# Performance work log

Measured on AMD Instinct MI355X. Metric: run time of the kernel, lower is better.

Reference implementation:

```python
import jax, jax.numpy as jnp
import numpy as np

N_NODES = 100000
N_EDGES = 1600000
HIDDEN = 64
IN_CH = 6  # 3 (direction) + 3 (node feature part)
BN_EPS = 1e-5


def setup_inputs() -> dict:
    key = jax.random.key(0)
    ks = jax.random.split(key, 16)
    inp = {
        "x": jax.random.normal(ks[0], (N_NODES, 3), dtype=jnp.float32),
        "pos": jax.random.normal(ks[1], (N_NODES, 3), dtype=jnp.float32),
        "edge_index": jax.random.randint(ks[2], (2, N_EDGES), 0, N_NODES, dtype=jnp.int64),
    }
    dims = [IN_CH, HIDDEN, HIDDEN, HIDDEN]
    for i in range(3):
        din, dout = dims[i], dims[i + 1]
        inp[f"W{i+1}"] = jax.random.normal(ks[3 + 4 * i], (din, dout), dtype=jnp.float32) * (1.0 / np.sqrt(din))
        inp[f"b{i+1}"] = jnp.zeros((dout,), dtype=jnp.float32)
        inp[f"g{i+1}"] = jnp.ones((dout,), dtype=jnp.float32)   # BN gamma
        inp[f"be{i+1}"] = jnp.zeros((dout,), dtype=jnp.float32)  # BN beta
    return inp


def _mlp_layer(h, W, b, g, be):
    # Linear -> ReLU -> BatchNorm1d (training mode, biased variance like torch)
    h = jax.nn.relu(h @ W + b)
    mu = jnp.mean(h, axis=0)
    var = jnp.mean((h - mu) ** 2, axis=0)
    return g * (h - mu) * jax.lax.rsqrt(var + BN_EPS) + be


def reference(x, pos, edge_index, W1, b1, g1, be1, W2, b2, g2, be2, W3, b3, g3, be3):
    n = x.shape[0]
    xp = jnp.concatenate([pos, x], axis=1)             # [N, 3+F]
    src, dst = edge_index[0], edge_index[1]            # j = src, i = dst (PyG source_to_target)
    x_j = xp[src]                                      # [E, 3+F]
    x_i = xp[dst]
    direction = x_j[:, :3] - x_i[:, :3]                # [E, 3]
    # NOTE: source uses torch.norm with no dim => single global scalar norm
    direction = direction / jnp.linalg.norm(direction)
    h = jnp.concatenate([direction, x_i[:, 3:]], axis=-1)  # [E, IN_CH]
    h = _mlp_layer(h, W1, b1, g1, be1)
    h = _mlp_layer(h, W2, b2, g2, be2)
    h = _mlp_layer(h, W3, b3, g3, be3)                 # [E, HIDDEN]
    out = jax.ops.segment_max(h, dst, num_segments=n)  # scatter-max aggregation
    out = jnp.where(jnp.isfinite(out), out, 0.0)       # PyG fills empty segments with 0
    return out
```

## Files before the change

### kernel.cpp

```cpp
#include <hip/hip_runtime.h>
#include <stdint.h>

typedef unsigned char u8;
typedef unsigned short u16;
typedef unsigned int u32;
typedef __attribute__((ext_vector_type(8))) short short8;
typedef __attribute__((ext_vector_type(4))) float floatx4;

#define BN_EPS 1e-5f
#define NPB 64
#define NPB_SHIFT 6
#define NBMAX 2048

__device__ __forceinline__ float bf2f(u16 u) { return __uint_as_float(((unsigned)u) << 16); }
__device__ __forceinline__ u16 f2bf(float f) {
  unsigned u = __float_as_uint(f);
  u += 0x7FFFu + ((u >> 16) & 1u);
  return (u16)(u >> 16);
}

__global__ void k_init(float* __restrict__ stats, u32* __restrict__ bucketTotal) {
  for (int i = threadIdx.x; i < 1024; i += blockDim.x) stats[i] = 0.f;
  for (int i = threadIdx.x; i < NBMAX + 1; i += blockDim.x) bucketTotal[i] = 0u;
}

__global__ void k_norm_hist(const int* __restrict__ ei, const float* __restrict__ pos,
                            int E, int NB, float* __restrict__ stats,
                            u32* __restrict__ bucketTotal) {
  __shared__ u32 lh[NBMAX];
  __shared__ float red[16];
  for (int i = threadIdx.x; i < NB; i += blockDim.x) lh[i] = 0u;
  __syncthreads();
  int tid = blockIdx.x * blockDim.x + threadIdx.x;
  int stride = gridDim.x * blockDim.x;
  float acc = 0.f;
  for (int e = tid; e < E; e += stride) {
    int s = ei[e], d = ei[E + e];
    float d0 = pos[3 * s + 0] - pos[3 * d + 0];
    float d1 = pos[3 * s + 1] - pos[3 * d + 1];
    float d2 = pos[3 * s + 2] - pos[3 * d + 2];
    acc = fmaf(d0, d0, acc);
    acc = fmaf(d1, d1, acc);
    acc = fmaf(d2, d2, acc);
    atomicAdd(&lh[d >> NPB_SHIFT], 1u);
  }
#pragma unroll
  for (int off = 32; off > 0; off >>= 1) acc += __shfl_down(acc, off, 64);
  if ((threadIdx.x & 63) == 0) red[threadIdx.x >> 6] = acc;
  __syncthreads();
  if (threadIdx.x == 0) {
    float s = 0.f;
    for (int w = 0; w < (int)(blockDim.x >> 6); w++) s += red[w];
    atomicAdd(&stats[0], s);
  }
  for (int i = threadIdx.x; i < NB; i += blockDim.x)
    if (lh[i]) atomicAdd(&bucketTotal[i], lh[i]);
}

__global__ void k_scan(const u32* __restrict__ bucketTotal, u32* __restrict__ base,
                       u32* __restrict__ cursor, int NB) {
  int lane = threadIdx.x;
  u32 run = 0;
  for (int b0 = 0; b0 < NB; b0 += 64) {
    int b = b0 + lane;
    u32 v = (b < NB) ? bucketTotal[b] : 0u;
    u32 s = v;
#pragma unroll
    for (int off = 1; off < 64; off <<= 1) {
      u32 t = __shfl_up(s, off, 64);
      if (lane >= off) s += t;
    }
    u32 excl = run + s - v;
    if (b < NB) { base[b] = excl; cursor[b] = excl; }
    run += __shfl(s, 63, 64);
  }
  if (lane == 0) base[NB] = run;
}

__global__ void k_place(const int* __restrict__ ei, int E, int NB,
                        u32* __restrict__ cursor, uint2* __restrict__ sorted2,
                        u8* __restrict__ ln8) {
  __shared__ u32 lh[NBMAX];
  __shared__ u32 lbase[NBMAX];
  for (int i = threadIdx.x; i < NB; i += blockDim.x) lh[i] = 0u;
  __syncthreads();
  int tid = blockIdx.x * blockDim.x + threadIdx.x;
  int stride = gridDim.x * blockDim.x;
  for (int e = tid; e < E; e += stride) atomicAdd(&lh[ei[E + e] >> NPB_SHIFT], 1u);
  __syncthreads();
  for (int i = threadIdx.x; i < NB; i += blockDim.x) {
    u32 c = lh[i];
    lbase[i] = c ? atomicAdd(&cursor[i], c) : 0u;
    lh[i] = 0u;
  }
  __syncthreads();
  for (int e = tid; e < E; e += stride) {
    int s = ei[e];
    int d = ei[E + e];
    int b = d >> NPB_SHIFT;
    u32 slot = lbase[b] + atomicAdd(&lh[b], 1u);
    sorted2[slot] = make_uint2((u32)s, (u32)d);
    ln8[slot] = (u8)(d & (NPB - 1));
  }
}

__global__ __launch_bounds__(256) void k_layer1(
    const int* __restrict__ ei, const float* __restrict__ pos,
    const float* __restrict__ x, const float* __restrict__ W1,
    const float* __restrict__ b1, u16* __restrict__ h,
    const float* __restrict__ stats, float* __restrict__ gsum,
    float* __restrict__ gsq, int E, const uint2* __restrict__ sorted2) {
  __shared__ float in6[6][256];
  __shared__ float ssum[64], ssq[64];
  float invn = 1.0f / sqrtf(stats[0]);
  int t = threadIdx.x;
  int lane = t & 63;
  int wv = t >> 6;
  int eslot = lane >> 3;
  int c0 = (lane & 7) * 8;
  float w[6][8];
#pragma unroll
  for (int k = 0; k < 6; k++)
#pragma unroll
    for (int j = 0; j < 8; j++) w[k][j] = W1[k * 64 + c0 + j];
  float bias[8];
#pragma unroll
  for (int j = 0; j < 8; j++) bias[j] = b1[c0 + j];
  float psum[8] = {0.f, 0.f, 0.f, 0.f, 0.f, 0.f, 0.f, 0.f};
  float psq[8] = {0.f, 0.f, 0.f, 0.f, 0.f, 0.f, 0.f, 0.f};

  int chunks = (E + 255) >> 8;
  for (int c = blockIdx.x; c < chunks; c += gridDim.x) {
    long e0 = (long)c << 8;
    int e = (int)e0 + t;
    float v[6] = {0.f, 0.f, 0.f, 0.f, 0.f, 0.f};
    if (e < E) {
      int s, d;
      if (sorted2) {
        uint2 sd = sorted2[e];
        s = (int)sd.x;
        d = (int)sd.y;
      } else {
        s = ei[e];
        d = ei[E + e];
      }
      float p0 = pos[3 * s + 0], p1 = pos[3 * s + 1], p2 = pos[3 * s + 2];
      float q0 = pos[3 * d + 0], q1 = pos[3 * d + 1], q2 = pos[3 * d + 2];
      v[0] = (p0 - q0) * invn;
      v[1] = (p1 - q1) * invn;
      v[2] = (p2 - q2) * invn;
      v[3] = x[3 * d + 0];
      v[4] = x[3 * d + 1];
      v[5] = x[3 * d + 2];
    }
    __syncthreads();
#pragma unroll
    for (int k = 0; k < 6; k++) in6[k][t] = v[k];
    __syncthreads();
    int lim = E - (int)e0;
    if (lim > 256) lim = 256;
#pragma unroll
    for (int i = 0; i < 8; i++) {
      int el = wv * 64 + i * 8 + eslot;
      if (el >= lim) continue;
      float hv[8];
#pragma unroll
      for (int j = 0; j < 8; j++) {
        float acc = bias[j];
#pragma unroll
        for (int k = 0; k < 6; k++) acc = fmaf(in6[k][el], w[k][j], acc);
        hv[j] = fmaxf(acc, 0.f);
      }
      u32 pk[4];
#pragma unroll
      for (int p = 0; p < 4; p++) {
        u16 lo = f2bf(hv[2 * p]);
        u16 hi = f2bf(hv[2 * p + 1]);
        pk[p] = (u32)lo | ((u32)hi << 16);
        float f0 = bf2f(lo), f1 = bf2f(hi);
        psum[2 * p] += f0;
        psq[2 * p] = fmaf(f0, f0, psq[2 * p]);
        psum[2 * p + 1] += f1;
        psq[2 * p + 1] = fmaf(f1, f1, psq[2 * p + 1]);
      }
      *(uint4*)(h + (e0 + el) * 64 + c0) = make_uint4(pk[0], pk[1], pk[2], pk[3]);
    }
  }
  if (t < 64) { ssum[t] = 0.f; ssq[t] = 0.f; }
  __syncthreads();
#pragma unroll
  for (int j = 0; j < 8; j++) {
    atomicAdd(&ssum[c0 + j], psum[j]);
    atomicAdd(&ssq[c0 + j], psq[j]);
  }
  __syncthreads();
  if (t < 64) {
    atomicAdd(&gsum[t], ssum[t]);
    atomicAdd(&gsq[t], ssq[t]);
  }
}

__global__ __launch_bounds__(256) void k_layer_mfma(
    u16* h, const float* __restrict__ W, const float* __restrict__ b,
    const float* __restrict__ gsum_in, const float* __restrict__ gsq_in,
    const float* __restrict__ g_in, const float* __restrict__ be_in, float invE,
    float* __restrict__ gsum, float* __restrict__ gsq, int E) {
  __shared__ float sc_s[64], sh_s[64];
  if (threadIdx.x < 64) {
    int c = threadIdx.x;
    float mu = gsum_in[c] * invE;
    float var = gsq_in[c] * invE - mu * mu;
    float s = g_in[c] * rsqrtf(var + BN_EPS);
    sc_s[c] = s;
    sh_s[c] = be_in[c] - mu * s;
  }
  __syncthreads();

  int lane = threadIdx.x & 63;
  int m = lane & 15;
  int q = lane >> 4;

  short8 bf[4][2];
  float bias[4];
#pragma unroll
  for (int t = 0; t < 4; t++) {
    int n = t * 16 + m;
    float bb = b[n];
    for (int k = 0; k < 64; k++) bb = fmaf(sh_s[k], W[k * 64 + n], bb);
    bias[t] = bb;
#pragma unroll
    for (int s = 0; s < 2; s++)
#pragma unroll
      for (int j = 0; j < 8; j++) {
        int k = s * 32 + q * 8 + j;
        bf[t][s][j] = (short)f2bf(W[k * 64 + n] * sc_s[k]);
      }
  }

  float psum[4] = {0.f, 0.f, 0.f, 0.f}, psq[4] = {0.f, 0.f, 0.f, 0.f};

  int tiles = E >> 4;
  int gw = ((int)blockIdx.x * (blockDim.x >> 6)) + (threadIdx.x >> 6);
  int nw = (int)gridDim.x * (blockDim.x >> 6);

  for (int tile = gw; tile < tiles; tile += nw) {
    long e0 = (long)tile * 16;
    const u16* rowp = h + (e0 + m) * 64 + q * 8;
    short8 a0 = *(const short8*)(rowp);
    short8 a1 = *(const short8*)(rowp + 32);
    floatx4 acc[4];
#pragma unroll
    for (int t = 0; t < 4; t++) acc[t] = (floatx4){0.f, 0.f, 0.f, 0.f};
#pragma unroll
    for (int t = 0; t < 4; t++)
      acc[t] = __builtin_amdgcn_mfma_f32_16x16x32_bf16(a0, bf[t][0], acc[t], 0, 0, 0);
#pragma unroll
    for (int t = 0; t < 4; t++)
      acc[t] = __builtin_amdgcn_mfma_f32_16x16x32_bf16(a1, bf[t][1], acc[t], 0, 0, 0);

#pragma unroll
    for (int t = 0; t < 4; t++) {
#pragma unroll
      for (int r = 0; r < 4; r++) {
        float v = acc[t][r] + bias[t];
        v = fmaxf(v, 0.f);
        u16 hb = f2bf(v);
        h[(e0 + q * 4 + r) * 64 + t * 16 + m] = hb;
        float hf = bf2f(hb);
        psum[t] += hf;
        psq[t] = fmaf(hf, hf, psq[t]);
      }
    }
  }

#pragma unroll
  for (int t = 0; t < 4; t++) {
    psum[t] += __shfl_xor(psum[t], 16, 64);
    psum[t] += __shfl_xor(psum[t], 32, 64);
    psq[t] += __shfl_xor(psq[t], 16, 64);
    psq[t] += __shfl_xor(psq[t], 32, 64);
  }
  __shared__ float ssum[64], ssq[64];
  if (threadIdx.x < 64) { ssum[threadIdx.x] = 0.f; ssq[threadIdx.x] = 0.f; }
  __syncthreads();
  if (q == 0) {
#pragma unroll
    for (int t = 0; t < 4; t++) {
      atomicAdd(&ssum[t * 16 + m], psum[t]);
      atomicAdd(&ssq[t * 16 + m], psq[t]);
    }
  }
  __syncthreads();
  if (threadIdx.x < 64) {
    atomicAdd(&gsum[threadIdx.x], ssum[threadIdx.x]);
    atomicAdd(&gsq[threadIdx.x], ssq[threadIdx.x]);
  }
}

__global__ __launch_bounds__(256) void k_bucket_max(
    const u8* __restrict__ ln8, const u32* __restrict__ base,
    const u16* __restrict__ h, const float* __restrict__ gsum3,
    const float* __restrict__ gsq3, const float* __restrict__ g3,
    const float* __restrict__ be3, float invE, float* __restrict__ outf, int N) {
  __shared__ u32 tile[NPB * 64];
  for (int i = threadIdx.x; i < NPB * 64; i += blockDim.x) tile[i] = 0u;
  int b = blockIdx.x;
  u32 start = base[b];
  int cnt = (int)(base[b + 1] - start);
  int t = threadIdx.x;
  int es = t >> 3;
  int c0 = (t & 7) * 8;
  u32 mm[4];
#pragma unroll
  for (int p = 0; p < 4; p++) {
    u32 m0 = (g3[c0 + 2 * p] < 0.f) ? 0xFFFFu : 0u;
    u32 m1 = (g3[c0 + 2 * p + 1] < 0.f) ? 0xFFFFu : 0u;
    mm[p] = m0 | (m1 << 16);
  }
  __syncthreads();

  for (int i0 = 0; i0 < cnt; i0 += 128) {
    uint4 raw[4];
    u32 ln[4];
    int ok[4];
#pragma unroll
    for (int u_ = 0; u_ < 4; u_++) {
      int sl = i0 + u_ * 32 + es;
      ok[u_] = sl < cnt;
      if (ok[u_]) {
        ln[u_] = (u32)ln8[start + sl];
        raw[u_] = *(const uint4*)(h + (long)(start + sl) * 64 + c0);
      }
    }
#pragma unroll
    for (int u_ = 0; u_ < 4; u_++) {
      if (!ok[u_]) continue;
      unsigned w[4] = {raw[u_].x, raw[u_].y, raw[u_].z, raw[u_].w};
      u32 key[8];
#pragma unroll
      for (int p = 0; p < 4; p++) {
        u32 wx = w[p] ^ mm[p];
        key[2 * p] = (wx & 0xFFFFu) | 0x10000u;
        key[2 * p + 1] = (wx >> 16) | 0x10000u;
      }
      u32 baseA = ln[u_] * 64u + (u32)c0;
#pragma unroll
      for (int jj = 0; jj < 8; jj++) {
        int j = (jj + es) & 7;
        atomicMax(&tile[baseA + j], key[j]);
      }
    }
  }
  __syncthreads();
  int c = t & 63;
  float mu = gsum3[c] * invE;
  float var = gsq3[c] * invE - mu * mu;
  float sc = g3[c] * rsqrtf(var + BN_EPS);
  float sh = be3[c] - mu * sc;
  u32 me = (g3[c] < 0.f) ? 0xFFFFu : 0u;
  int node0 = b * NPB;
  for (int l = t; l < NPB * 64; l += blockDim.x) {
    int node = node0 + (l >> 6);
    if (node < N) {
      u32 k = tile[l];
      float v = (k == 0u) ? 0.f : fmaf(bf2f((u16)((k & 0xFFFFu) ^ me)), sc, sh);
      outf[(long)node * 64 + (l & 63)] = v;
    }
  }
}

__global__ void k_initout(float* __restrict__ outf, long n, float* __restrict__ stats,
                          u32* __restrict__ bucketTotal) {
  long i = (long)blockIdx.x * blockDim.x + threadIdx.x;
  long stride = (long)gridDim.x * blockDim.x;
  for (long j = i; j < n; j += stride) outf[j] = __uint_as_float(0xFF800000u);
  if (i < 1024) stats[i] = 0.f;
  if (i < NBMAX + 1) bucketTotal[i] = 0u;
}
__global__ void k_scatter(const int* __restrict__ ei, const u16* __restrict__ h,
                          const float* __restrict__ gsum3, const float* __restrict__ gsq3,
                          const float* __restrict__ g3, const float* __restrict__ be3,
                          float invE, float* outf, int E) {
  int lane = threadIdx.x & 63;
  int gw = ((int)blockIdx.x * (blockDim.x >> 6)) + (threadIdx.x >> 6);
  int nw = (int)gridDim.x * (blockDim.x >> 6);
  float mu = gsum3[lane] * invE;
  float var = gsq3[lane] * invE - mu * mu;
  float sc = g3[lane] * rsqrtf(var + BN_EPS);
  float sh = be3[lane] - mu * sc;
  for (int e = gw; e < E; e += nw) {
    int d = ei[E + e];
    float v = fmaf(bf2f(h[(long)e * 64 + lane]), sc, sh);
    float* addr = outf + (long)d * 64 + lane;
    if (v >= 0.f)
      atomicMax((int*)addr, __float_as_int(v));
    else
      atomicMin((unsigned int*)addr, __float_as_uint(v));
  }
}
__global__ void k_out(float* __restrict__ outf, long n) {
  long i = (long)blockIdx.x * blockDim.x + threadIdx.x;
  long stride = (long)gridDim.x * blockDim.x;
  for (long j = i; j < n; j += stride) {
    float v = outf[j];
    unsigned u = __float_as_uint(v);
    if ((u & 0x7F800000u) == 0x7F800000u) v = 0.f;
    outf[j] = v;
  }
}

extern "C" void kernel_launch(void* const* d_in, const int* in_sizes, int n_in,
                              void* d_out, int out_size, void* d_ws, size_t ws_size,
                              hipStream_t stream) {
  const float* x = (const float*)d_in[0];
  const float* pos = (const float*)d_in[1];
  const int* ei = (const int*)d_in[2];
  const float* W1 = (const float*)d_in[3];
  const float* b1 = (const float*)d_in[4];
  const float* g1 = (const float*)d_in[5];
  const float* be1 = (const float*)d_in[6];
  const float* W2 = (const float*)d_in[7];
  const float* b2 = (const float*)d_in[8];
  const float* g2 = (const float*)d_in[9];
  const float* be2 = (const float*)d_in[10];
  const float* W3 = (const float*)d_in[11];
  const float* b3 = (const float*)d_in[12];
  const float* g3 = (const float*)d_in[13];
  const float* be3 = (const float*)d_in[14];

  int N = in_sizes[0] / 3;
  int E = in_sizes[2] / 2;
  int NB = (N + NPB - 1) / NPB;
  long n_out = (long)N * 64;

  char* wsb = (char*)d_ws;
  u16* h = (u16*)wsb;
  size_t off = (size_t)E * 64 * 2;
  float* stats = (float*)(wsb + off);
  off += 1024 * 4;
  u32* bucketTotal = (u32*)(wsb + off);
  off += (NBMAX + 1) * 4;
  u32* baseArr = (u32*)(wsb + off);
  off += (NBMAX + 1) * 4;
  u32* cursor = (u32*)(wsb + off);
  off += NBMAX * 4;
  off = (off + 7) & ~(size_t)7;
  uint2* sorted2 = (uint2*)(wsb + off);
  off += (size_t)E * 8;
  u8* ln8 = (u8*)(wsb + off);
  off += (size_t)E;
  size_t need = off;

  float* gsum1 = stats + 64, * gsq1 = stats + 128;
  float* gsum2 = stats + 192, * gsq2 = stats + 256;
  float* gsum3 = stats + 320, * gsq3 = stats + 384;

  float* outf = (float*)d_out;
  float invE = 1.0f / (float)E;
  bool binned = (ws_size >= need) && (NB <= NBMAX);

  if (binned) {
    k_init<<<1, 1024, 0, stream>>>(stats, bucketTotal);
    k_norm_hist<<<256, 256, 0, stream>>>(ei, pos, E, NB, stats, bucketTotal);
    k_scan<<<1, 64, 0, stream>>>(bucketTotal, baseArr, cursor, NB);
    k_place<<<256, 256, 0, stream>>>(ei, E, NB, cursor, sorted2, ln8);
    k_layer1<<<1024, 256, 0, stream>>>(ei, pos, x, W1, b1, h, stats, gsum1, gsq1, E, sorted2);
    k_layer_mfma<<<2048, 256, 0, stream>>>(h, W2, b2, gsum1, gsq1, g1, be1, invE, gsum2, gsq2, E);
    k_layer_mfma<<<2048, 256, 0, stream>>>(h, W3, b3, gsum2, gsq2, g2, be2, invE, gsum3, gsq3, E);
    k_bucket_max<<<NB, 256, 0, stream>>>(ln8, baseArr, h, gsum3, gsq3, g3, be3, invE, outf, N);
  } else {
    k_initout<<<4096, 256, 0, stream>>>(outf, n_out, stats, bucketTotal);
    k_norm_hist<<<256, 256, 0, stream>>>(ei, pos, E, NB <= NBMAX ? NB : 1, stats, bucketTotal);
    k_layer1<<<1024, 256, 0, stream>>>(ei, pos, x, W1, b1, h, stats, gsum1, gsq1, E, (const uint2*)nullptr);
    k_layer_mfma<<<2048, 256, 0, stream>>>(h, W2, b2, gsum1, gsq1, g1, be1, invE, gsum2, gsq2, E);
    k_layer_mfma<<<2048, 256, 0, stream>>>(h, W3, b3, gsum2, gsq2, g2, be2, invE, gsum3, gsq3, E);
    k_scatter<<<2048, 256, 0, stream>>>(ei, h, gsum3, gsq3, g3, be3, invE, outf, E);
    k_out<<<2048, 256, 0, stream>>>(outf, n_out);
  }
}
```

Before: 500.3 us.

## Fuse layer1 and layer2 by recomputing layer1 after a stats-only pass

Replaces the layer1 kernel that wrote bf16 activations to memory with a stats-only pass that computes BN1 statistics without storing h. A new fused kernel then recomputes layer1 per edge, stages it in shared memory, folds the BN1 scale and shift into W2 and b2, and runs the layer2 MFMA directly. This avoids one full E×64 bf16 write and read of the intermediate activations, at the cost of gathering pos and x twice and recomputing the small 6→64 layer. Grid sizes for the fused kernel and the layer3 kernel also change.

Result: slower. 515.0 us (+2.9%).

```diff
diff --git a/kernel.cpp b/kernel.cpp
--- a/kernel.cpp
+++ b/kernel.cpp
@@ -101,6 +101,247 @@
     u32 slot = lbase[b] + atomicAdd(&lh[b], 1u);
     sorted2[slot] = make_uint2((u32)s, (u32)d);
     ln8[slot] = (u8)(d & (NPB - 1));
+  }
+}
+
+__global__ __launch_bounds__(256) void k_stats1(
+    const float* __restrict__ pos, const float* __restrict__ x,
+    const float* __restrict__ W1, const float* __restrict__ b1,
+    const float* __restrict__ stats, float* __restrict__ gsum,
+    float* __restrict__ gsq, int E, const uint2* __restrict__ sorted2) {
+  __shared__ float in6[6][256];
+  __shared__ float ssum[64], ssq[64];
+  float invn = 1.0f / sqrtf(stats[0]);
+  int t = threadIdx.x;
+  int lane = t & 63;
+  int wv = t >> 6;
+  int eslot = lane >> 3;
+  int c0 = (lane & 7) * 8;
+  float w[6][8];
+#pragma unroll
+  for (int k = 0; k < 6; k++)
+#pragma unroll
+    for (int j = 0; j < 8; j++) w[k][j] = W1[k * 64 + c0 + j];
+  float bias[8];
+#pragma unroll
+  for (int j = 0; j < 8; j++) bias[j] = b1[c0 + j];
+  float psum[8] = {0.f, 0.f, 0.f, 0.f, 0.f, 0.f, 0.f, 0.f};
+  float psq[8] = {0.f, 0.f, 0.f, 0.f, 0.f, 0.f, 0.f, 0.f};
+
+  int chunks = (E + 255) >> 8;
+  for (int c = blockIdx.x; c < chunks; c += gridDim.x) {
+    long e0 = (long)c << 8;
+    int e = (int)e0 + t;
+    float v[6] = {0.f, 0.f, 0.f, 0.f, 0.f, 0.f};
+    if (e < E) {
+      uint2 sd = sorted2[e];
+      int s = (int)sd.x, d = (int)sd.y;
+      float p0 = pos[3 * s + 0], p1 = pos[3 * s + 1], p2 = pos[3 * s + 2];
+      float q0 = pos[3 * d + 0], q1 = pos[3 * d + 1], q2 = pos[3 * d + 2];
+      v[0] = (p0 - q0) * invn;
+      v[1] = (p1 - q1) * invn;
+      v[2] = (p2 - q2) * invn;
+      v[3] = x[3 * d + 0];
+      v[4] = x[3 * d + 1];
+      v[5] = x[3 * d + 2];
+    }
+    __syncthreads();
+#pragma unroll
+    for (int k = 0; k < 6; k++) in6[k][t] = v[k];
+    __syncthreads();
+    int lim = E - (int)e0;
+    if (lim > 256) lim = 256;
+#pragma unroll
+    for (int i = 0; i < 8; i++) {
+      int el = wv * 64 + i * 8 + eslot;
+      if (el >= lim) continue;
+      float inr[6];
+#pragma unroll
+      for (int k = 0; k < 6; k++) inr[k] = in6[k][el];
+#pragma unroll
+      for (int j = 0; j < 8; j++) {
+        float acc = bias[j];
+#pragma unroll
+        for (int k = 0; k < 6; k++) acc = fmaf(inr[k], w[k][j], acc);
+        float hf = bf2f(f2bf(fmaxf(acc, 0.f)));
+        psum[j] += hf;
+        psq[j] = fmaf(hf, hf, psq[j]);
+      }
+    }
+  }
+  if (t < 64) { ssum[t] = 0.f; ssq[t] = 0.f; }
+  __syncthreads();
+#pragma unroll
+  for (int j = 0; j < 8; j++) {
+    atomicAdd(&ssum[c0 + j], psum[j]);
+    atomicAdd(&ssq[c0 + j], psq[j]);
+  }
+  __syncthreads();
+  if (t < 64) {
+    atomicAdd(&gsum[t], ssum[t]);
+    atomicAdd(&gsq[t], ssq[t]);
+  }
+}
+
+__global__ __launch_bounds__(256) void k_layer12(
+    const float* __restrict__ pos, const float* __restrict__ x,
+    const float* __restrict__ W1, const float* __restrict__ b1,
+    const float* __restrict__ stats, const uint2* __restrict__ sorted2,
+    const float* __restrict__ W2, const float* __restrict__ b2,
+    const float* __restrict__ gsum_in, const float* __restrict__ gsq_in,
+    const float* __restrict__ g_in, const float* __restrict__ be_in,
+    float invE, u16* __restrict__ h, float* __restrict__ gsum,
+    float* __restrict__ gsq, int E) {
+  __shared__ float sc_s[64], sh_s[64];
+  __shared__ float w1s[384];
+  __shared__ float b1s[64];
+  __shared__ float in6[6][256];
+  __shared__ __attribute__((aligned(16))) u16 stage[256 * 64];
+  __shared__ float ssum[64], ssq[64];
+
+  if (threadIdx.x < 64) {
+    int c = threadIdx.x;
+    float mu = gsum_in[c] * invE;
+    float var = gsq_in[c] * invE - mu * mu;
+    float s = g_in[c] * rsqrtf(var + BN_EPS);
+    sc_s[c] = s;
+    sh_s[c] = be_in[c] - mu * s;
+    b1s[c] = b1[c];
+  }
+  for (int i = threadIdx.x; i < 384; i += blockDim.x) w1s[i] = W1[i];
+  __syncthreads();
+
+  int lane = threadIdx.x & 63;
+  int m = lane & 15;
+  int q = lane >> 4;
+  int wv = threadIdx.x >> 6;
+  int eslot = lane >> 3;
+  int c0 = (lane & 7) * 8;
+
+  short8 bf[4][2];
+  float bias2[4];
+#pragma unroll
+  for (int t = 0; t < 4; t++) {
+    int n = t * 16 + m;
+    float bb = b2[n];
+    for (int k = 0; k < 64; k++) bb = fmaf(sh_s[k], W2[k * 64 + n], bb);
+    bias2[t] = bb;
+#pragma unroll
+    for (int s = 0; s < 2; s++)
+#pragma unroll
+      for (int j = 0; j < 8; j++) {
+        int k = s * 32 + q * 8 + j;
+        bf[t][s][j] = (short)f2bf(W2[k * 64 + n] * sc_s[k]);
+      }
+  }
+
+  float invn = 1.0f / sqrtf(stats[0]);
+  float psum[4] = {0.f, 0.f, 0.f, 0.f}, psq[4] = {0.f, 0.f, 0.f, 0.f};
+
+  int chunks = (E + 255) >> 8;
+  for (int c = blockIdx.x; c < chunks; c += gridDim.x) {
+    long e0 = (long)c << 8;
+    int e = (int)e0 + threadIdx.x;
+    float v[6] = {0.f, 0.f, 0.f, 0.f, 0.f, 0.f};
+    if (e < E) {
+      uint2 sd = sorted2[e];
+      int s = (int)sd.x, d = (int)sd.y;
+      float p0 = pos[3 * s + 0], p1 = pos[3 * s + 1], p2 = pos[3 * s + 2];
+      float q0 = pos[3 * d + 0], q1 = pos[3 * d + 1], q2 = pos[3 * d + 2];
+      v[0] = (p0 - q0) * invn;
+      v[1] = (p1 - q1) * invn;
+      v[2] = (p2 - q2) * invn;
+      v[3] = x[3 * d + 0];
+      v[4] = x[3 * d + 1];
+      v[5] = x[3 * d + 2];
+    }
+    __syncthreads();
+#pragma unroll
+    for (int k = 0; k < 6; k++) in6[k][threadIdx.x] = v[k];
+    __syncthreads();
+    int lim = E - (int)e0;
+    if (lim > 256) lim = 256;
+#pragma unroll
+    for (int i = 0; i < 8; i++) {
+      int el = wv * 64 + i * 8 + eslot;
+      u32 pk[4] = {0u, 0u, 0u, 0u};
+      if (el < lim) {
+        float inr[6];
+#pragma unroll
+        for (int k = 0; k < 6; k++) inr[k] = in6[k][el];
+#pragma unroll
+        for (int p = 0; p < 4; p++) {
+          float a0f = b1s[c0 + 2 * p];
+          float a1f = b1s[c0 + 2 * p + 1];
+#pragma unroll
+          for (int k = 0; k < 6; k++) {
+            a0f = fmaf(inr[k], w1s[k * 64 + c0 + 2 * p], a0f);
+            a1f = fmaf(inr[k], w1s[k * 64 + c0 + 2 * p + 1], a1f);
+          }
+          u16 lo = f2bf(fmaxf(a0f, 0.f));
+          u16 hi = f2bf(fmaxf(a1f, 0.f));
+          pk[p] = (u32)lo | ((u32)hi << 16);
+        }
+      }
+      int sl = (lane & 7) ^ (el & 7);
+      *(uint4*)(stage + el * 64 + sl * 8) = make_uint4(pk[0], pk[1], pk[2], pk[3]);
+    }
+    __syncthreads();
+#pragma unroll
+    for (int tt = 0; tt < 4; tt++) {
+      int tl = wv * 4 + tt;
+      int el2 = tl * 16 + m;
+      const u16* rp = stage + el2 * 64;
+      short8 a0 = *(const short8*)(rp + ((q ^ (m & 7)) << 3));
+      short8 a1 = *(const short8*)(rp + (((4 + q) ^ (m & 7)) << 3));
+      floatx4 acc[4];
+#pragma unroll
+      for (int t = 0; t < 4; t++) acc[t] = (floatx4){0.f, 0.f, 0.f, 0.f};
+#pragma unroll
+      for (int t = 0; t < 4; t++)
+        acc[t] = __builtin_amdgcn_mfma_f32_16x16x32_bf16(a0, bf[t][0], acc[t], 0, 0, 0);
+#pragma unroll
+      for (int t = 0; t < 4; t++)
+        acc[t] = __builtin_amdgcn_mfma_f32_16x16x32_bf16(a1, bf[t][1], acc[t], 0, 0, 0);
+#pragma unroll
+      for (int t = 0; t < 4; t++) {
+#pragma unroll
+        for (int r = 0; r < 4; r++) {
+          int er = tl * 16 + q * 4 + r;
+          if (er < lim) {
+            float vv = acc[t][r] + bias2[t];
+            vv = fmaxf(vv, 0.f);
+            u16 hb = f2bf(vv);
+            h[(e0 + er) * 64 + t * 16 + m] = hb;
+            float hf = bf2f(hb);
+            psum[t] += hf;
+            psq[t] = fmaf(hf, hf, psq[t]);
+          }
+        }
+      }
+    }
+  }
+
+#pragma unroll
+  for (int t = 0; t < 4; t++) {
+    psum[t] += __shfl_xor(psum[t], 16, 64);
+    psum[t] += __shfl_xor(psum[t], 32, 64);
+    psq[t] += __shfl_xor(psq[t], 16, 64);
+    psq[t] += __shfl_xor(psq[t], 32, 64);
+  }
+  if (threadIdx.x < 64) { ssum[threadIdx.x] = 0.f; ssq[threadIdx.x] = 0.f; }
+  __syncthreads();
+  if (q == 0) {
+#pragma unroll
+    for (int t = 0; t < 4; t++) {
+      atomicAdd(&ssum[t * 16 + m], psum[t]);
+      atomicAdd(&ssq[t * 16 + m], psq[t]);
+    }
+  }
+  __syncthreads();
+  if (threadIdx.x < 64) {
+    atomicAdd(&gsum[threadIdx.x], ssum[threadIdx.x]);
+    atomicAdd(&gsq[threadIdx.x], ssq[threadIdx.x]);
   }
 }
 
@@ -464,9 +705,10 @@
     k_norm_hist<<<256, 256, 0, stream>>>(ei, pos, E, NB, stats, bucketTotal);
     k_scan<<<1, 64, 0, stream>>>(bucketTotal, baseArr, cursor, NB);
     k_place<<<256, 256, 0, stream>>>(ei, E, NB, cursor, sorted2, ln8);
-    k_layer1<<<1024, 256, 0, stream>>>(ei, pos, x, W1, b1, h, stats, gsum1, gsq1, E, sorted2);
-    k_layer_mfma<<<2048, 256, 0, stream>>>(h, W2, b2, gsum1, gsq1, g1, be1, invE, gsum2, gsq2, E);
-    k_layer_mfma<<<2048, 256, 0, stream>>>(h, W3, b3, gsum2, gsq2, g2, be2, invE, gsum3, gsq3, E);
+    k_stats1<<<1024, 256, 0, stream>>>(pos, x, W1, b1, stats, gsum1, gsq1, E, sorted2);
+    k_layer12<<<768, 256, 0, stream>>>(pos, x, W1, b1, stats, sorted2, W2, b2,
+                                       gsum1, gsq1, g1, be1, invE, h, gsum2, gsq2, E);
+    k_layer_mfma<<<1536, 256, 0, stream>>>(h, W3, b3, gsum2, gsq2, g2, be2, invE, gsum3, gsq3, E);
     k_bucket_max<<<NB, 256, 0, stream>>>(ln8, baseArr, h, gsum3, gsq3, g3, be3, invE, outf, N);
   } else {
     k_initout<<<4096, 256, 0, stream>>>(outf, n_out, stats, bucketTotal);
```
